# Kernel optimization log

Hardware: AMD Instinct MI355X
Metric: run time of the kernel (lower is better)

## Reference

```python
import jax, jax.numpy as jnp
import numpy as np

N = 100000        # nodes
E_HALF = 1600000  # directed edges before symmetrization
NFEAT, NHID, NOUT = 512, 256, 64
K = 10            # Chebyshev order


def setup_inputs() -> dict:
    key = jax.random.key(0)
    k_feat, k_src, k_dst, k_w1, k_w2, k_tmp = jax.random.split(key, 6)
    feature = jax.random.normal(k_feat, (N, NFEAT), jnp.float32)
    src = jax.random.randint(k_src, (E_HALF,), 0, N, jnp.int32)
    dst = jax.random.randint(k_dst, (E_HALF,), 0, N, jnp.int32)
    # symmetrize so the adjacency (and hence the normalized Laplacian) is symmetric
    edge_index = jnp.stack([jnp.concatenate([src, dst]), jnp.concatenate([dst, src])])  # [2, 2*E_HALF]
    W1 = jax.random.normal(k_w1, (NHID, NFEAT), jnp.float32) / np.sqrt(NFEAT)
    b1 = jnp.zeros((NHID,), jnp.float32)
    W2 = jax.random.normal(k_w2, (NOUT, NHID), jnp.float32) / np.sqrt(NHID)
    b2 = jnp.zeros((NOUT,), jnp.float32)
    # ChebnetII_prop.temp is initialized to 1.0; jitter so relu/grads are non-trivial
    temp = 1.0 + 0.1 * jax.random.normal(k_tmp, (K + 1,), jnp.float32)
    return {"feature": feature, "W1": W1, "b1": b1, "W2": W2, "b2": b2,
            "temp": temp, "edge_index": edge_index}


def _cheb_coeffs(temp):
    # coe[i] = 2/(K+1) * sum_j relu(temp)[j] * T_i(x_j),  x_j = cos((K-j+0.5)*pi/(K+1))
    # and T_i(cos(theta)) = cos(i*theta)
    coe_tmp = jax.nn.relu(temp)
    j = jnp.arange(K + 1, dtype=temp.dtype)
    theta = (K - j + 0.5) * jnp.pi / (K + 1)          # [K+1]
    i = jnp.arange(K + 1, dtype=temp.dtype)
    T = jnp.cos(i[:, None] * theta[None, :])           # [K+1, K+1] Chebyshev eval table
    return (2.0 / (K + 1)) * (T @ coe_tmp)             # [K+1]


def reference(feature, W1, b1, W2, b2, temp, edge_index):
    # dense MLP part (dropout is identity in eval mode)
    x = jax.nn.relu(feature @ W1.T + b1)               # [N, NHID]
    x = x @ W2.T + b2                                  # [N, NOUT]

    # ChebnetII_prop: propagate with L_tilde = L_sym - I = -D^{-1/2} A D^{-1/2}
    row, col = edge_index[0], edge_index[1]
    w = jnp.ones(row.shape, x.dtype)                   # unit edge weights (binary adjacency)
    deg = jax.ops.segment_sum(w, row, num_segments=N)  # [N]
    dinv = jnp.where(deg > 0, jax.lax.rsqrt(jnp.maximum(deg, 1.0)), 0.0)
    norm = -dinv[row] * w * dinv[col]                  # [E] edge weights of (L - I)

    def prop(v):  # v: [N, NOUT] -> (L - I) @ v via gather/scatter
        return jax.ops.segment_sum(norm[:, None] * v[col], row, num_segments=N)

    coe = _cheb_coeffs(temp)
    Tx0 = x
    Tx1 = prop(x)
    out = coe[0] / 2.0 * Tx0 + coe[1] * Tx1
    for i in range(2, K + 1):                          # Chebyshev recursion (K fixed, small)
        Tx2 = 2.0 * prop(Tx1) - Tx0
        out = out + coe[i] * Tx2
        Tx0, Tx1 = Tx1, Tx2
    return out                                         # [N, NOUT]
```

## Files before the change

kernel.cpp:

```cpp
#include <hip/hip_runtime.h>

#define K_ORDER 10
#define NFEAT 512
#define NHID 256
#define NOUT 64
#define PI_F 3.14159265358979323846f
#define SCAN_CHUNK 2048

typedef __bf16 bf16x8 __attribute__((ext_vector_type(8)));
typedef unsigned short ushort8 __attribute__((ext_vector_type(8)));
typedef float f32x4 __attribute__((ext_vector_type(4)));

__device__ __forceinline__ float bf2f(unsigned short u) {
    union { unsigned int i; float f; } x;
    x.i = ((unsigned int)u) << 16;
    return x.f;
}

__device__ __forceinline__ unsigned short f2bfu(float f) {
    __bf16 h = (__bf16)f;
    return *(unsigned short*)&h;
}

#define GLOAD_LDS16(g, l) __builtin_amdgcn_global_load_lds( \
    (const __attribute__((address_space(1))) void*)(g),     \
    (__attribute__((address_space(3))) void*)(l), 16, 0, 0)

__global__ void detect_kernel(const unsigned short* __restrict__ temp, int* __restrict__ flag) {
    if (threadIdx.x == 0 && blockIdx.x == 0) {
        int cnt = 0;
        for (int i = 0; i < K_ORDER + 1; ++i) {
            unsigned short s = temp[i];
            if (s >= 0x3E00 && s < 0x4080) cnt++;
        }
        flag[0] = (cnt >= 9) ? 1 : 0;
    }
}

__global__ void prep_weights(const void* __restrict__ W1, const void* __restrict__ b1,
                             const void* __restrict__ W2, const void* __restrict__ b2,
                             const int* __restrict__ flag,
                             unsigned short* __restrict__ w1o, float* __restrict__ b1o,
                             unsigned short* __restrict__ w2o, float* __restrict__ b2o) {
    bool isbf = flag[0] != 0;
    int stride = gridDim.x * blockDim.x;
    int i0 = blockIdx.x * blockDim.x + threadIdx.x;
    const int n1 = NHID * NFEAT;
    const int n2 = NOUT * NHID;
    for (int i = i0; i < n1; i += stride)
        w1o[i] = isbf ? ((const unsigned short*)W1)[i] : f2bfu(((const float*)W1)[i]);
    for (int i = i0; i < n2; i += stride)
        w2o[i] = isbf ? ((const unsigned short*)W2)[i] : f2bfu(((const float*)W2)[i]);
    for (int i = i0; i < NHID; i += stride)
        b1o[i] = isbf ? bf2f(((const unsigned short*)b1)[i]) : ((const float*)b1)[i];
    for (int i = i0; i < NOUT; i += stride)
        b2o[i] = isbf ? bf2f(((const unsigned short*)b2)[i]) : ((const float*)b2)[i];
}


__global__ void count_deg_kernel(const int* __restrict__ row, int* __restrict__ deg, int e) {
    int i = blockIdx.x * blockDim.x + threadIdx.x;
    if (i < e) atomicAdd(&deg[row[i]], 1);
}

__global__ void dinv_kernel(const int* __restrict__ deg, float* __restrict__ dinv, int n) {
    int i = blockIdx.x * blockDim.x + threadIdx.x;
    if (i < n) {
        int d = deg[i];
        dinv[i] = (d > 0) ? rsqrtf((float)d) : 0.0f;
    }
}

__global__ __launch_bounds__(256) void partial_sum_kernel(const int* __restrict__ deg,
                                                          int* __restrict__ bsum, int n) {
    __shared__ int ws[4];
    int b = blockIdx.x, t = threadIdx.x;
    int base = b * SCAN_CHUNK + t * 8;
    int s = 0;
    #pragma unroll
    for (int j = 0; j < 8; ++j) { int i = base + j; if (i < n) s += deg[i]; }
    #pragma unroll
    for (int m = 1; m < 64; m <<= 1) s += __shfl_xor(s, m, 64);
    if ((t & 63) == 0) ws[t >> 6] = s;
    __syncthreads();
    if (t == 0) bsum[b] = ws[0] + ws[1] + ws[2] + ws[3];
}

__global__ void scan_small_kernel(const int* __restrict__ bsum, int* __restrict__ boff,
                                  int* __restrict__ rowptr, int nb, int n) {
    int t = threadIdx.x;
    int v = (t < nb) ? bsum[t] : 0;
    int x = v;
    #pragma unroll
    for (int m = 1; m < 64; m <<= 1) { int y = __shfl_up(x, m, 64); if (t >= m) x += y; }
    if (t < nb) boff[t] = x - v;
    if (t == 63) rowptr[n] = x;
}

__global__ __launch_bounds__(256) void scan_apply_kernel(const int* __restrict__ deg,
                                                         const int* __restrict__ boff,
                                                         int* __restrict__ rowptr,
                                                         int* __restrict__ cursor, int n) {
    __shared__ int wtot[4];
    __shared__ int woff_s[4];
    int b = blockIdx.x, t = threadIdx.x;
    int lane = t & 63, wid = t >> 6;
    int base = b * SCAN_CHUNK + t * 8;
    int v[8], s[8];
    int run = 0;
    #pragma unroll
    for (int j = 0; j < 8; ++j) {
        int i = base + j;
        v[j] = (i < n) ? deg[i] : 0;
        run += v[j];
        s[j] = run;
    }
    int tsum = run;
    int x = tsum;
    #pragma unroll
    for (int m = 1; m < 64; m <<= 1) { int y = __shfl_up(x, m, 64); if (lane >= m) x += y; }
    int texcl = x - tsum;
    if (lane == 63) wtot[wid] = x;
    __syncthreads();
    if (t == 0) {
        int r = 0;
        #pragma unroll
        for (int w = 0; w < 4; ++w) { woff_s[w] = r; r += wtot[w]; }
    }
    __syncthreads();
    int ebase = boff[b] + woff_s[wid] + texcl;
    #pragma unroll
    for (int j = 0; j < 8; ++j) {
        int i = base + j;
        if (i < n) { int ex = ebase + s[j] - v[j]; rowptr[i] = ex; cursor[i] = ex; }
    }
}

__global__ void part_bounds_kernel(const int* __restrict__ rowptr, int* __restrict__ pb,
                                   int n, int e) {
    int j = threadIdx.x;
    if (j > 8) return;
    if (j == 8) { pb[8] = n; return; }
    long target = (long)j * e / 8;
    int lo = 0, hi = n;
    while (lo < hi) {
        int mid = (lo + hi) >> 1;
        if ((long)rowptr[mid] < target) lo = mid + 1; else hi = mid;
    }
    pb[j] = lo;
}

__global__ __launch_bounds__(256) void scatter_part_kernel(
    const int* __restrict__ row, const int* __restrict__ col,
    const int* __restrict__ pbounds, int* __restrict__ cursor,
    int* __restrict__ cols_s, int e) {
    const int j = blockIdx.x & 7;
    const int lo = pbounds[j], hi = pbounds[j + 1];
    const int base = ((blockIdx.x >> 3) * 256 + threadIdx.x) * 4;
    if (base + 3 < e) {
        int4 r4 = *(const int4*)(row + base);
        int4 c4 = *(const int4*)(col + base);
        #pragma unroll
        for (int k = 0; k < 4; ++k) {
            int r = (&r4.x)[k];
            if (r >= lo && r < hi) {
                int p = atomicAdd(&cursor[r], 1);
                cols_s[p] = (&c4.x)[k];
            }
        }
    } else {
        for (int k = 0; k < 4; ++k) {
            int i = base + k;
            if (i < e) {
                int r = row[i];
                if (r >= lo && r < hi) {
                    int p = atomicAdd(&cursor[r], 1);
                    cols_s[p] = col[i];
                }
            }
        }
    }
}


__global__ void coef_kernel(const void* __restrict__ temp, const int* __restrict__ flag,
                            float* __restrict__ coe) {
    int i = threadIdx.x;
    bool isbf = flag[0] != 0;
    if (i <= K_ORDER) {
        float s = 0.0f;
        #pragma unroll
        for (int j = 0; j <= K_ORDER; ++j) {
            float t = isbf ? bf2f(((const unsigned short*)temp)[j]) : ((const float*)temp)[j];
            t = fmaxf(t, 0.0f);
            float theta = ((float)(K_ORDER - j) + 0.5f) * PI_F / (float)(K_ORDER + 1);
            s += cosf((float)i * theta) * t;
        }
        coe[i] = (2.0f / (float)(K_ORDER + 1)) * s;
    }
}


template<int BN, int NBY, bool RELU, bool A_FLAGGED>
__global__ __launch_bounds__(256) void gemm_kernel(
    const void* __restrict__ A, const unsigned short* __restrict__ Bw,
    const float* __restrict__ bias, const int* __restrict__ flag,
    unsigned short* __restrict__ C, int M, int Kdim, int ldc)
{
    constexpr int BM = 128, BK = 32;
    constexpr int FN = BN / 32;
    constexpr int ABUF = A_FLAGGED ? (BM * BK * 4) : (BM * BK * 2);
    constexpr int BBUF = BN * BK * 2;
    __shared__ char lds[2 * ABUF + 2 * BBUF] __attribute__((aligned(16)));

    const int tid = threadIdx.x;
    const int lane = tid & 63, wid = tid >> 6;
    const int bid = blockIdx.x;
    const int by = bid % NBY;
    const int bx = bid / NBY;
    const int row0 = bx * BM;
    const int col0 = by * BN;
    const int wrow = (wid >> 1) * (BM / 2);
    const int wcol = (wid & 1) * (BN / 2);
    const bool af32 = A_FLAGGED ? (flag[0] == 0) : false;

    char* ldsA0 = lds;
    char* ldsB0 = lds + 2 * ABUF;

    auto stage = [&](int buf, int k0) {
        {
            constexpr int PW = (BBUF / 1024) / 4;
            #pragma unroll
            for (int rr = 0; rr < PW; ++rr) {
                int q = rr * 4 + wid;
                int off = q * 1024 + lane * 16;
                int brow = off >> 6;
                int scol = ((off >> 4) & 3) ^ (brow & 3);
                const char* src = (const char*)Bw + (((size_t)(col0 + brow) * Kdim + k0) << 1) + scol * 16;
                GLOAD_LDS16(src, ldsB0 + buf * BBUF + q * 1024);
            }
        }
        if (af32) {
            #pragma unroll
            for (int rr = 0; rr < 4; ++rr) {
                int q = rr * 4 + wid;
                int off = q * 1024 + lane * 16;
                int arow = off >> 7;
                int scol = ((off >> 4) & 7) ^ (arow & 7);
                int grow = row0 + arow; if (grow >= M) grow = M - 1;
                const char* src = (const char*)A + (((size_t)grow * Kdim + k0) << 2) + scol * 16;
                GLOAD_LDS16(src, ldsA0 + buf * ABUF + q * 1024);
            }
        } else {
            #pragma unroll
            for (int rr = 0; rr < 2; ++rr) {
                int q = rr * 4 + wid;
                int off = q * 1024 + lane * 16;
                int arow = off >> 6;
                int scol = ((off >> 4) & 3) ^ (arow & 3);
                int grow = row0 + arow; if (grow >= M) grow = M - 1;
                const char* src = (const char*)A + (((size_t)grow * Kdim + k0) << 1) + scol * 16;
                GLOAD_LDS16(src, ldsA0 + buf * ABUF + q * 1024);
            }
        }
    };

    f32x4 acc[4][FN] = {};

    auto compute = [&](int buf) {
        const char* Ab = ldsA0 + buf * ABUF;
        const char* Bb = ldsB0 + buf * BBUF;
        const int kq = lane >> 4;
        bf16x8 af[4];
        if (af32) {
            #pragma unroll
            for (int mi = 0; mi < 4; ++mi) {
                int aRow = wrow + mi * 16 + (lane & 15);
                int base = aRow * 128 + kq * 32;
                int sw = (aRow & 7) << 4;
                f32x4 lo = *(const f32x4*)(Ab + (base ^ sw));
                f32x4 hi = *(const f32x4*)(Ab + ((base + 16) ^ sw));
                #pragma unroll
                for (int j = 0; j < 4; ++j) { af[mi][j] = (__bf16)lo[j]; af[mi][j + 4] = (__bf16)hi[j]; }
            }
        } else {
            #pragma unroll
            for (int mi = 0; mi < 4; ++mi) {
                int aRow = wrow + mi * 16 + (lane & 15);
                int o = (aRow * 64 + kq * 16) ^ ((aRow & 3) << 4);
                af[mi] = *(const bf16x8*)(Ab + o);
            }
        }
        bf16x8 bfv[FN];
        #pragma unroll
        for (int ni = 0; ni < FN; ++ni) {
            int bRow = wcol + ni * 16 + (lane & 15);
            int o = (bRow * 64 + kq * 16) ^ ((bRow & 3) << 4);
            bfv[ni] = *(const bf16x8*)(Bb + o);
        }
        #pragma unroll
        for (int mi = 0; mi < 4; ++mi)
            #pragma unroll
            for (int ni = 0; ni < FN; ++ni)
                acc[mi][ni] = __builtin_amdgcn_mfma_f32_16x16x32_bf16(af[mi], bfv[ni],
                                                                      acc[mi][ni], 0, 0, 0);
    };

    const int NT = Kdim / BK;
    stage(0, 0);
    __syncthreads();
    int buf = 0;
    for (int t = 0; t < NT; ++t) {
        if (t + 1 < NT) stage(buf ^ 1, (t + 1) * BK);
        compute(buf);
        __syncthreads();
        buf ^= 1;
    }

    #pragma unroll
    for (int mi = 0; mi < 4; ++mi) {
        #pragma unroll
        for (int ni = 0; ni < FN; ++ni) {
            #pragma unroll
            for (int rg = 0; rg < 4; ++rg) {
                int grow = row0 + wrow + mi * 16 + (lane >> 4) * 4 + rg;
                int gcol = col0 + wcol + ni * 16 + (lane & 15);
                if (grow < M) {
                    float vv = acc[mi][ni][rg] + bias[gcol];
                    if (RELU) vv = fmaxf(vv, 0.0f);
                    C[(size_t)grow * ldc + gcol] = f2bfu(vv);
                }
            }
        }
    }
}


__global__ __launch_bounds__(256) void prop_kernel(const unsigned short* __restrict__ vsrc,
                                                   unsigned short* __restrict__ tdst,
                                                   float* __restrict__ outacc,
                                                   const int* __restrict__ rowptr,
                                                   const int* __restrict__ cols,
                                                   const float* __restrict__ dinv,
                                                   const float* __restrict__ coe,
                                                   int mode, int ci, int n) {
    int lane = threadIdx.x & 63;
    int r = blockIdx.x * 4 + (threadIdx.x >> 6);
    if (r >= n) return;
    int fc = lane & 7;
    int sub = lane >> 3;
    int e0 = rowptr[r], e1 = rowptr[r + 1];
    float acc[8] = {};
    for (int e = e0; e < e1; e += 8) {
        int ee = e + sub;
        bool valid = ee < e1;
        int c = valid ? cols[ee] : 0;
        float w = valid ? dinv[c] : 0.0f;
        ushort8 vv = *(const ushort8*)&vsrc[(size_t)c * NOUT + fc * 8];
        #pragma unroll
        for (int j = 0; j < 8; ++j)
            acc[j] = fmaf(w, bf2f(vv[j]), acc[j]);
    }
    #pragma unroll
    for (int m = 8; m < 64; m <<= 1)
        #pragma unroll
        for (int j = 0; j < 8; ++j)
            acc[j] += __shfl_xor(acc[j], m, 64);

    if (lane < 8) {
        float dr = -dinv[r];
        size_t idx = (size_t)r * NOUT + lane * 8;
        float P[8];
        #pragma unroll
        for (int j = 0; j < 8; ++j) P[j] = dr * acc[j];
        if (mode == 0) {
            ushort8 v0 = *(const ushort8*)&vsrc[idx];
            ushort8 hout;
            #pragma unroll
            for (int j = 0; j < 8; ++j) {
                __bf16 h = (__bf16)P[j];
                hout[j] = *(unsigned short*)&h;
            }
            *(ushort8*)&tdst[idx] = hout;
            #pragma unroll
            for (int j = 0; j < 8; ++j)
                outacc[idx + j] = coe[0] * 0.5f * bf2f(v0[j]) + coe[1] * P[j];
        } else {
            ushort8 t0v = *(const ushort8*)&tdst[idx];
            ushort8 hout;
            float t2a[8];
            #pragma unroll
            for (int j = 0; j < 8; ++j) {
                float t2 = 2.0f * P[j] - bf2f(t0v[j]);
                t2a[j] = t2;
                __bf16 h = (__bf16)t2;
                hout[j] = *(unsigned short*)&h;
            }
            *(ushort8*)&tdst[idx] = hout;
            #pragma unroll
            for (int j = 0; j < 8; ++j)
                outacc[idx + j] += coe[ci] * t2a[j];
        }
    }
}

__global__ void convert_kernel(const float* __restrict__ in, const int* __restrict__ flag,
                               void* __restrict__ out, int n) {
    int i = blockIdx.x * blockDim.x + threadIdx.x;
    bool isbf = flag[0] != 0;
    if (i < n) {
        float v = in[i];
        if (isbf) {
            __bf16 h = (__bf16)v;
            ((unsigned short*)out)[i] = *(unsigned short*)&h;
        } else {
            ((float*)out)[i] = v;
        }
    }
}


extern "C" void kernel_launch(void* const* d_in, const int* in_sizes, int n_in,
                              void* d_out, int out_size, void* d_ws, size_t ws_size,
                              hipStream_t stream) {
    const void* feature = d_in[0];
    const void* W1      = d_in[1];
    const void* b1      = d_in[2];
    const void* W2      = d_in[3];
    const void* b2      = d_in[4];
    const void* temp    = d_in[5];
    const int* edge_index = (const int*)d_in[6];

    const int N = in_sizes[0] / NFEAT;
    const int E = in_sizes[6] / 2;
    const int* row = edge_index;
    const int* col = edge_index + E;
    const int nb = (N + SCAN_CHUNK - 1) / SCAN_CHUNK;

    char* base = (char*)d_ws;
    size_t off = 0;
    auto alloc = [&](size_t bytes) -> char* {
        char* p = base + off;
        off = (off + bytes + 255) & ~(size_t)255;
        return p;
    };
    int*   flag   = (int*)  alloc(4);
    float* coe    = (float*)alloc(64);
    int*   bsum   = (int*)  alloc(256);
    int*   boff   = (int*)  alloc(256);
    int*   pbounds= (int*)  alloc(64);
    unsigned short* w1c = (unsigned short*)alloc((size_t)NHID * NFEAT * 2);
    float* b1c    = (float*)alloc(NHID * 4);
    unsigned short* w2c = (unsigned short*)alloc((size_t)NOUT * NHID * 2);
    float* b2c    = (float*)alloc(NOUT * 4);
    float* dinv   = (float*)alloc((size_t)N * 4);
    int*   deg    = (int*)  alloc((size_t)N * 4);
    int*   rowptr = (int*)  alloc((size_t)(N + 1) * 4);
    int*   cursor = (int*)  alloc((size_t)(N + 1) * 4);
    char*  R      = alloc((size_t)N * NHID * 2);
    unsigned short* xhid = (unsigned short*)R;
    int*   colss  = (int*)R;
    float* outacc = (float*)(R + (size_t)E * 4);
    unsigned short* t_a = (unsigned short*)alloc((size_t)N * NOUT * 2);
    unsigned short* t_b = (unsigned short*)alloc((size_t)N * NOUT * 2);

    detect_kernel<<<1, 64, 0, stream>>>((const unsigned short*)temp, flag);
    coef_kernel<<<1, 64, 0, stream>>>(temp, flag, coe);
    prep_weights<<<128, 256, 0, stream>>>(W1, b1, W2, b2, flag, w1c, b1c, w2c, b2c);

    const int nbm = (N + 127) / 128;
    gemm_kernel<128, 2, true, true><<<dim3(nbm * 2), 256, 0, stream>>>(
        feature, w1c, b1c, flag, xhid, N, NFEAT, NHID);
    gemm_kernel<64, 1, false, false><<<dim3(nbm), 256, 0, stream>>>(
        xhid, w2c, b2c, flag, t_a, N, NHID, NOUT);

    hipMemsetAsync(deg, 0, (size_t)N * 4, stream);
    count_deg_kernel<<<(E + 255) / 256, 256, 0, stream>>>(row, deg, E);
    dinv_kernel<<<(N + 255) / 256, 256, 0, stream>>>(deg, dinv, N);
    partial_sum_kernel<<<nb, 256, 0, stream>>>(deg, bsum, N);
    scan_small_kernel<<<1, 64, 0, stream>>>(bsum, boff, rowptr, nb, N);
    scan_apply_kernel<<<nb, 256, 0, stream>>>(deg, boff, rowptr, cursor, N);
    part_bounds_kernel<<<1, 16, 0, stream>>>(rowptr, pbounds, N, E);
    {
        int nch = (E + 1023) / 1024;
        scatter_part_kernel<<<nch * 8, 256, 0, stream>>>(row, col, pbounds, cursor, colss, E);
    }

    int pb = (N + 3) / 4;
    prop_kernel<<<pb, 256, 0, stream>>>(t_a, t_b, outacc, rowptr, colss, dinv, coe, 0, 0, N);
    unsigned short* src = t_b;
    unsigned short* dst = t_a;
    for (int i = 2; i <= K_ORDER; ++i) {
        prop_kernel<<<pb, 256, 0, stream>>>(src, dst, outacc, rowptr, colss, dinv, coe, 1, i, N);
        unsigned short* tmp = src; src = dst; dst = tmp;
    }

    convert_kernel<<<(N * NOUT + 255) / 256, 256, 0, stream>>>(outacc, flag, d_out, N * NOUT);
}
```

Before: 1.427 ms.

## Bin CSR columns by source range, pack dinv with column, unroll gather

```diff
diff --git a/kernel.cpp b/kernel.cpp
--- a/kernel.cpp
+++ b/kernel.cpp
@@ -6,6 +6,8 @@
 #define NOUT 64
 #define PI_F 3.14159265358979323846f
 #define SCAN_CHUNK 2048
+#define NRANGE 8
+#define RSHIFT 14
 
 typedef __bf16 bf16x8 __attribute__((ext_vector_type(8)));
 typedef unsigned short ushort8 __attribute__((ext_vector_type(8)));
@@ -58,16 +60,21 @@
 }
 
 
-__global__ void count_deg_kernel(const int* __restrict__ row, int* __restrict__ deg, int e) {
+__global__ void countb_kernel(const int* __restrict__ row, const int* __restrict__ col,
+                              int* __restrict__ degb, int e) {
     int i = blockIdx.x * blockDim.x + threadIdx.x;
-    if (i < e) atomicAdd(&deg[row[i]], 1);
-}
-
-__global__ void dinv_kernel(const int* __restrict__ deg, float* __restrict__ dinv, int n) {
-    int i = blockIdx.x * blockDim.x + threadIdx.x;
-    if (i < n) {
-        int d = deg[i];
-        dinv[i] = (d > 0) ? rsqrtf((float)d) : 0.0f;
+    if (i < e) atomicAdd(&degb[(size_t)row[i] * NRANGE + (col[i] >> RSHIFT)], 1);
+}
+
+__global__ void sumdeg_kernel(const int* __restrict__ degb, int* __restrict__ deg,
+                              float* __restrict__ dinv, int n) {
+    int r = blockIdx.x * blockDim.x + threadIdx.x;
+    if (r < n) {
+        int4 a = *(const int4*)&degb[(size_t)r * NRANGE];
+        int4 b = *(const int4*)&degb[(size_t)r * NRANGE + 4];
+        int d = a.x + a.y + a.z + a.w + b.x + b.y + b.z + b.w;
+        deg[r] = d;
+        dinv[r] = (d > 0) ? rsqrtf((float)d) : 0.0f;
     }
 }
 
@@ -136,6 +143,26 @@
     }
 }
 
+__global__ void binoff_kernel(const int* __restrict__ degb, const int* __restrict__ rowptr,
+                              int* __restrict__ cursor_b, int n) {
+    int r = blockIdx.x * blockDim.x + threadIdx.x;
+    if (r >= n) return;
+    int4 a = *(const int4*)&degb[(size_t)r * NRANGE];
+    int4 b = *(const int4*)&degb[(size_t)r * NRANGE + 4];
+    int run = rowptr[r];
+    int4 o0, o1;
+    o0.x = run; run += a.x;
+    o0.y = run; run += a.y;
+    o0.z = run; run += a.z;
+    o0.w = run; run += a.w;
+    o1.x = run; run += b.x;
+    o1.y = run; run += b.y;
+    o1.z = run; run += b.z;
+    o1.w = run;
+    *(int4*)&cursor_b[(size_t)r * NRANGE] = o0;
+    *(int4*)&cursor_b[(size_t)r * NRANGE + 4] = o1;
+}
+
 __global__ void part_bounds_kernel(const int* __restrict__ rowptr, int* __restrict__ pb,
                                    int n, int e) {
     int j = threadIdx.x;
@@ -152,8 +179,8 @@
 
 __global__ __launch_bounds__(256) void scatter_part_kernel(
     const int* __restrict__ row, const int* __restrict__ col,
-    const int* __restrict__ pbounds, int* __restrict__ cursor,
-    int* __restrict__ cols_s, int e) {
+    const int* __restrict__ pbounds, const float* __restrict__ dinv,
+    int* __restrict__ cursor_b, int2* __restrict__ pairs, int e) {
     const int j = blockIdx.x & 7;
     const int lo = pbounds[j], hi = pbounds[j + 1];
     const int base = ((blockIdx.x >> 3) * 256 + threadIdx.x) * 4;
@@ -164,8 +191,9 @@
         for (int k = 0; k < 4; ++k) {
             int r = (&r4.x)[k];
             if (r >= lo && r < hi) {
-                int p = atomicAdd(&cursor[r], 1);
-                cols_s[p] = (&c4.x)[k];
+                int c = (&c4.x)[k];
+                int p = atomicAdd(&cursor_b[(size_t)r * NRANGE + (c >> RSHIFT)], 1);
+                pairs[p] = make_int2(c, __float_as_int(dinv[c]));
             }
         }
     } else {
@@ -174,8 +202,9 @@
             if (i < e) {
                 int r = row[i];
                 if (r >= lo && r < hi) {
-                    int p = atomicAdd(&cursor[r], 1);
-                    cols_s[p] = col[i];
+                    int c = col[i];
+                    int p = atomicAdd(&cursor_b[(size_t)r * NRANGE + (c >> RSHIFT)], 1);
+                    pairs[p] = make_int2(c, __float_as_int(dinv[c]));
                 }
             }
         }
@@ -340,7 +369,7 @@
                                                    unsigned short* __restrict__ tdst,
                                                    float* __restrict__ outacc,
                                                    const int* __restrict__ rowptr,
-                                                   const int* __restrict__ cols,
+                                                   const int2* __restrict__ pairs,
                                                    const float* __restrict__ dinv,
                                                    const float* __restrict__ coe,
                                                    int mode, int ci, int n) {
@@ -351,15 +380,23 @@
     int sub = lane >> 3;
     int e0 = rowptr[r], e1 = rowptr[r + 1];
     float acc[8] = {};
-    for (int e = e0; e < e1; e += 8) {
-        int ee = e + sub;
-        bool valid = ee < e1;
-        int c = valid ? cols[ee] : 0;
-        float w = valid ? dinv[c] : 0.0f;
-        ushort8 vv = *(const ushort8*)&vsrc[(size_t)c * NOUT + fc * 8];
-        #pragma unroll
-        for (int j = 0; j < 8; ++j)
-            acc[j] = fmaf(w, bf2f(vv[j]), acc[j]);
+    for (int e = e0; e < e1; e += 32) {
+        int cc[4]; float ww[4];
+        #pragma unroll
+        for (int u = 0; u < 4; ++u) {
+            int ee = e + u * 8 + sub;
+            bool valid = ee < e1;
+            int2 pr = valid ? pairs[ee] : make_int2(0, 0);
+            cc[u] = pr.x;
+            ww[u] = __int_as_float(pr.y);
+        }
+        #pragma unroll
+        for (int u = 0; u < 4; ++u) {
+            ushort8 vv = *(const ushort8*)&vsrc[(size_t)cc[u] * NOUT + fc * 8];
+            #pragma unroll
+            for (int j = 0; j < 8; ++j)
+                acc[j] = fmaf(ww[u], bf2f(vv[j]), acc[j]);
+        }
     }
     #pragma unroll
     for (int m = 8; m < 64; m <<= 1)
@@ -436,6 +473,7 @@
     const int* row = edge_index;
     const int* col = edge_index + E;
     const int nb = (N + SCAN_CHUNK - 1) / SCAN_CHUNK;
+    const int nbin = N * NRANGE;
 
     char* base = (char*)d_ws;
     size_t off = 0;
@@ -457,10 +495,12 @@
     int*   deg    = (int*)  alloc((size_t)N * 4);
     int*   rowptr = (int*)  alloc((size_t)(N + 1) * 4);
     int*   cursor = (int*)  alloc((size_t)(N + 1) * 4);
+    int*   degb   = (int*)  alloc((size_t)nbin * 4);
+    int*   cursor_b = (int*)alloc((size_t)nbin * 4);
     char*  R      = alloc((size_t)N * NHID * 2);
     unsigned short* xhid = (unsigned short*)R;
-    int*   colss  = (int*)R;
-    float* outacc = (float*)(R + (size_t)E * 4);
+    int2*  pairs  = (int2*)R;
+    float* outacc = (float*)(R + (size_t)E * 8);
     unsigned short* t_a = (unsigned short*)alloc((size_t)N * NOUT * 2);
     unsigned short* t_b = (unsigned short*)alloc((size_t)N * NOUT * 2);
 
@@ -474,24 +514,26 @@
     gemm_kernel<64, 1, false, false><<<dim3(nbm), 256, 0, stream>>>(
         xhid, w2c, b2c, flag, t_a, N, NHID, NOUT);
 
-    hipMemsetAsync(deg, 0, (size_t)N * 4, stream);
-    count_deg_kernel<<<(E + 255) / 256, 256, 0, stream>>>(row, deg, E);
-    dinv_kernel<<<(N + 255) / 256, 256, 0, stream>>>(deg, dinv, N);
+    hipMemsetAsync(degb, 0, (size_t)nbin * 4, stream);
+    countb_kernel<<<(E + 255) / 256, 256, 0, stream>>>(row, col, degb, E);
+    sumdeg_kernel<<<(N + 255) / 256, 256, 0, stream>>>(degb, deg, dinv, N);
     partial_sum_kernel<<<nb, 256, 0, stream>>>(deg, bsum, N);
     scan_small_kernel<<<1, 64, 0, stream>>>(bsum, boff, rowptr, nb, N);
     scan_apply_kernel<<<nb, 256, 0, stream>>>(deg, boff, rowptr, cursor, N);
+    binoff_kernel<<<(N + 255) / 256, 256, 0, stream>>>(degb, rowptr, cursor_b, N);
     part_bounds_kernel<<<1, 16, 0, stream>>>(rowptr, pbounds, N, E);
     {
         int nch = (E + 1023) / 1024;
-        scatter_part_kernel<<<nch * 8, 256, 0, stream>>>(row, col, pbounds, cursor, colss, E);
+        scatter_part_kernel<<<nch * 8, 256, 0, stream>>>(row, col, pbounds, dinv,
+                                                         cursor_b, pairs, E);
     }
 
     int pb = (N + 3) / 4;
-    prop_kernel<<<pb, 256, 0, stream>>>(t_a, t_b, outacc, rowptr, colss, dinv, coe, 0, 0, N);
+    prop_kernel<<<pb, 256, 0, stream>>>(t_a, t_b, outacc, rowptr, pairs, dinv, coe, 0, 0, N);
     unsigned short* src = t_b;
     unsigned short* dst = t_a;
     for (int i = 2; i <= K_ORDER; ++i) {
-        prop_kernel<<<pb, 256, 0, stream>>>(src, dst, outacc, rowptr, colss, dinv, coe, 1, i, N);
+        prop_kernel<<<pb, 256, 0, stream>>>(src, dst, outacc, rowptr, pairs, dinv, coe, 1, i, N);
         unsigned short* tmp = src; src = dst; dst = tmp;
     }
 
```

After: 1.351 ms. 5.3% less time.

## Pack column and dinv into edge pairs, unroll gathers, use nontemporal accesses

Applied to the files above, without the earlier changes.

```diff
diff --git a/kernel.cpp b/kernel.cpp
--- a/kernel.cpp
+++ b/kernel.cpp
@@ -10,6 +10,7 @@
 typedef __bf16 bf16x8 __attribute__((ext_vector_type(8)));
 typedef unsigned short ushort8 __attribute__((ext_vector_type(8)));
 typedef float f32x4 __attribute__((ext_vector_type(4)));
+typedef unsigned int u32x4 __attribute__((ext_vector_type(4)));
 
 __device__ __forceinline__ float bf2f(unsigned short u) {
     union { unsigned int i; float f; } x;
@@ -152,8 +153,8 @@
 
 __global__ __launch_bounds__(256) void scatter_part_kernel(
     const int* __restrict__ row, const int* __restrict__ col,
-    const int* __restrict__ pbounds, int* __restrict__ cursor,
-    int* __restrict__ cols_s, int e) {
+    const int* __restrict__ pbounds, const float* __restrict__ dinv,
+    int* __restrict__ cursor, int2* __restrict__ pairs, int e) {
     const int j = blockIdx.x & 7;
     const int lo = pbounds[j], hi = pbounds[j + 1];
     const int base = ((blockIdx.x >> 3) * 256 + threadIdx.x) * 4;
@@ -164,8 +165,9 @@
         for (int k = 0; k < 4; ++k) {
             int r = (&r4.x)[k];
             if (r >= lo && r < hi) {
+                int c = (&c4.x)[k];
                 int p = atomicAdd(&cursor[r], 1);
-                cols_s[p] = (&c4.x)[k];
+                pairs[p] = make_int2(c, __float_as_int(dinv[c]));
             }
         }
     } else {
@@ -174,8 +176,9 @@
             if (i < e) {
                 int r = row[i];
                 if (r >= lo && r < hi) {
+                    int c = col[i];
                     int p = atomicAdd(&cursor[r], 1);
-                    cols_s[p] = col[i];
+                    pairs[p] = make_int2(c, __float_as_int(dinv[c]));
                 }
             }
         }
@@ -340,7 +343,7 @@
                                                    unsigned short* __restrict__ tdst,
                                                    float* __restrict__ outacc,
                                                    const int* __restrict__ rowptr,
-                                                   const int* __restrict__ cols,
+                                                   const int2* __restrict__ pairs,
                                                    const float* __restrict__ dinv,
                                                    const float* __restrict__ coe,
                                                    int mode, int ci, int n) {
@@ -351,15 +354,25 @@
     int sub = lane >> 3;
     int e0 = rowptr[r], e1 = rowptr[r + 1];
     float acc[8] = {};
-    for (int e = e0; e < e1; e += 8) {
-        int ee = e + sub;
-        bool valid = ee < e1;
-        int c = valid ? cols[ee] : 0;
-        float w = valid ? dinv[c] : 0.0f;
-        ushort8 vv = *(const ushort8*)&vsrc[(size_t)c * NOUT + fc * 8];
-        #pragma unroll
-        for (int j = 0; j < 8; ++j)
-            acc[j] = fmaf(w, bf2f(vv[j]), acc[j]);
+    for (int e = e0; e < e1; e += 32) {
+        int cc[4]; float ww[4];
+        #pragma unroll
+        for (int u = 0; u < 4; ++u) {
+            int ee = e + u * 8 + sub;
+            bool valid = ee < e1;
+            unsigned long long pv = valid
+                ? __builtin_nontemporal_load((const unsigned long long*)(pairs + ee))
+                : 0ull;
+            cc[u] = (int)(pv & 0xFFFFFFFFull);
+            ww[u] = valid ? __int_as_float((int)(pv >> 32)) : 0.0f;
+        }
+        #pragma unroll
+        for (int u = 0; u < 4; ++u) {
+            ushort8 vv = *(const ushort8*)&vsrc[(size_t)cc[u] * NOUT + fc * 8];
+            #pragma unroll
+            for (int j = 0; j < 8; ++j)
+                acc[j] = fmaf(ww[u], bf2f(vv[j]), acc[j]);
+        }
     }
     #pragma unroll
     for (int m = 8; m < 64; m <<= 1)
@@ -377,29 +390,39 @@
             ushort8 v0 = *(const ushort8*)&vsrc[idx];
             ushort8 hout;
             #pragma unroll
-            for (int j = 0; j < 8; ++j) {
-                __bf16 h = (__bf16)P[j];
-                hout[j] = *(unsigned short*)&h;
-            }
-            *(ushort8*)&tdst[idx] = hout;
-            #pragma unroll
-            for (int j = 0; j < 8; ++j)
-                outacc[idx + j] = coe[0] * 0.5f * bf2f(v0[j]) + coe[1] * P[j];
+            for (int j = 0; j < 8; ++j) hout[j] = f2bfu(P[j]);
+            __builtin_nontemporal_store(*(u32x4*)&hout, (u32x4*)&tdst[idx]);
+            float c0 = coe[0] * 0.5f, c1 = coe[1];
+            f32x4 lo, hi;
+            #pragma unroll
+            for (int j = 0; j < 4; ++j) {
+                lo[j] = c0 * bf2f(v0[j]) + c1 * P[j];
+                hi[j] = c0 * bf2f(v0[j + 4]) + c1 * P[j + 4];
+            }
+            __builtin_nontemporal_store(lo, (f32x4*)&outacc[idx]);
+            __builtin_nontemporal_store(hi, (f32x4*)&outacc[idx + 4]);
         } else {
-            ushort8 t0v = *(const ushort8*)&tdst[idx];
+            u32x4 tv = __builtin_nontemporal_load((const u32x4*)&tdst[idx]);
+            ushort8 t0v = *(ushort8*)&tv;
             ushort8 hout;
+            float cc2 = coe[ci];
             float t2a[8];
             #pragma unroll
             for (int j = 0; j < 8; ++j) {
                 float t2 = 2.0f * P[j] - bf2f(t0v[j]);
                 t2a[j] = t2;
-                __bf16 h = (__bf16)t2;
-                hout[j] = *(unsigned short*)&h;
-            }
-            *(ushort8*)&tdst[idx] = hout;
-            #pragma unroll
-            for (int j = 0; j < 8; ++j)
-                outacc[idx + j] += coe[ci] * t2a[j];
+                hout[j] = f2bfu(t2);
+            }
+            __builtin_nontemporal_store(*(u32x4*)&hout, (u32x4*)&tdst[idx]);
+            f32x4 lo = __builtin_nontemporal_load((const f32x4*)&outacc[idx]);
+            f32x4 hi = __builtin_nontemporal_load((const f32x4*)&outacc[idx + 4]);
+            #pragma unroll
+            for (int j = 0; j < 4; ++j) {
+                lo[j] += cc2 * t2a[j];
+                hi[j] += cc2 * t2a[j + 4];
+            }
+            __builtin_nontemporal_store(lo, (f32x4*)&outacc[idx]);
+            __builtin_nontemporal_store(hi, (f32x4*)&outacc[idx + 4]);
         }
     }
 }
@@ -459,8 +482,8 @@
     int*   cursor = (int*)  alloc((size_t)(N + 1) * 4);
     char*  R      = alloc((size_t)N * NHID * 2);
     unsigned short* xhid = (unsigned short*)R;
-    int*   colss  = (int*)R;
-    float* outacc = (float*)(R + (size_t)E * 4);
+    int2*  pairs  = (int2*)R;
+    float* outacc = (float*)(R + (size_t)E * 8);
     unsigned short* t_a = (unsigned short*)alloc((size_t)N * NOUT * 2);
     unsigned short* t_b = (unsigned short*)alloc((size_t)N * NOUT * 2);
 
@@ -483,15 +506,16 @@
     part_bounds_kernel<<<1, 16, 0, stream>>>(rowptr, pbounds, N, E);
     {
         int nch = (E + 1023) / 1024;
-        scatter_part_kernel<<<nch * 8, 256, 0, stream>>>(row, col, pbounds, cursor, colss, E);
+        scatter_part_kernel<<<nch * 8, 256, 0, stream>>>(row, col, pbounds, dinv,
+                                                         cursor, pairs, E);
     }
 
     int pb = (N + 3) / 4;
-    prop_kernel<<<pb, 256, 0, stream>>>(t_a, t_b, outacc, rowptr, colss, dinv, coe, 0, 0, N);
+    prop_kernel<<<pb, 256, 0, stream>>>(t_a, t_b, outacc, rowptr, pairs, dinv, coe, 0, 0, N);
     unsigned short* src = t_b;
     unsigned short* dst = t_a;
     for (int i = 2; i <= K_ORDER; ++i) {
-        prop_kernel<<<pb, 256, 0, stream>>>(src, dst, outacc, rowptr, colss, dinv, coe, 1, i, N);
+        prop_kernel<<<pb, 256, 0, stream>>>(src, dst, outacc, rowptr, pairs, dinv, coe, 1, i, N);
         unsigned short* tmp = src; src = dst; dst = tmp;
     }
 
```

Result: faster. 1.386 ms (-2.8%).
